# Optimization experiments

Hardware: AMD Instinct MI355X
Metric: run time of the kernel (lower is better)

## Reference

```python
import jax, jax.numpy as jnp
import numpy as np

B, T, N, D_IN = 2, 64, 64, 512
HID, L, H = 256, 2, 4
C = HID // H  # 64 per-head channels
NEG_SLOPE = 0.2
LN_EPS = 1e-5


def setup_inputs() -> dict:
    key = jax.random.key(0)
    ks = jax.random.split(key, 8)
    s_in = 1.0 / np.sqrt(D_IN)
    s_h = 1.0 / np.sqrt(HID)
    s_c = 1.0 / np.sqrt(C)
    return {
        "x": jax.random.normal(ks[0], (B, T, N, D_IN), jnp.float32),
        "person_mask": jax.random.randint(ks[1], (B, T, N), 0, 2) > 0,
        "W_in": (jax.random.normal(ks[2], (D_IN, HID)) * s_in).astype(jnp.float32),
        "b_in": jnp.zeros((HID,), jnp.float32),
        "Wl": (jax.random.normal(ks[3], (L, HID, HID)) * s_h).astype(jnp.float32),
        "bl": jnp.zeros((L, HID), jnp.float32),
        "Wr": (jax.random.normal(ks[4], (L, HID, HID)) * s_h).astype(jnp.float32),
        "br": jnp.zeros((L, HID), jnp.float32),
        "att": (jax.random.normal(ks[5], (L, H, C)) * s_c).astype(jnp.float32),
        "out_bias": jnp.zeros((L, HID), jnp.float32),
        "ln_scale": jnp.ones((L, HID), jnp.float32),
        "ln_bias": jnp.zeros((L, HID), jnp.float32),
    }


def _layernorm(x, g, b):
    mu = jnp.mean(x, axis=-1, keepdims=True)
    var = jnp.mean(jnp.square(x - mu), axis=-1, keepdims=True)
    return (x - mu) * jax.lax.rsqrt(var + LN_EPS) * g + b


def _gatv2_layer(h, allowed, Wl, bl, Wr, br, att, ob):
    # h: [bt, N, HID]; allowed: [bt, N, N] bool (edge j->i at [b,i,j])
    bt, n, _ = h.shape
    xl = (h @ Wl + bl).reshape(bt, n, H, C)  # source features (messages)
    xr = (h @ Wr + br).reshape(bt, n, H, C)  # target features
    # GATv2 logit: e_ij = a . leaky_relu(xr_i + xl_j), per head
    s = xr[:, :, None, :, :] + xl[:, None, :, :, :]  # [bt, i, j, H, C]
    e = jnp.einsum('bijhc,hc->bijh', jax.nn.leaky_relu(s, NEG_SLOPE), att)
    e = jnp.where(allowed[..., None], e, -1e9)
    alpha = jax.nn.softmax(e, axis=2)  # segment softmax over incoming edges j
    out = jnp.einsum('bijh,bjhc->bihc', alpha, xl)  # weighted scatter-sum
    return out.reshape(bt, n, H * C) + ob


def _forward(x, person_mask, W_in, b_in, Wl, bl, Wr, br, att, out_bias, ln_scale, ln_bias):
    b, t, n, _ = x.shape
    bt = b * t
    h = (x @ W_in + b_in).reshape(bt, n, HID)
    m = person_mask.reshape(bt, n)
    # edges: all pairs among masked nodes (incl. diag) + self loops for every node
    allowed = (m[:, :, None] & m[:, None, :]) | jnp.eye(n, dtype=bool)[None]
    hi = h
    for li in range(L):
        res = hi
        g = _gatv2_layer(hi, allowed, Wl[li], bl[li], Wr[li], br[li], att[li], out_bias[li])
        g = jax.nn.elu(g)  # dropout is identity in eval mode
        g = _layernorm(g, ln_scale[li], ln_bias[li])
        hi = g + res  # use_residual=True
        hi = jnp.where(m[:, :, None], hi, 0.0)
    # graphs with <=1 masked node are skipped (pass through projected features)
    keep = (jnp.sum(m, axis=-1) > 1)[:, None, None]
    out = jnp.where(keep, hi, h)
    return out.reshape(b, t, n, HID)


def reference(x, person_mask, W_in, b_in, Wl, bl, Wr, br, att, out_bias, ln_scale, ln_bias):
    return _forward(x, person_mask, W_in, b_in, Wl, bl, Wr, br, att, out_bias, ln_scale, ln_bias)
```

## Files before the change

kernel.cpp:

```cpp
#include <hip/hip_runtime.h>
#include <hip/hip_bf16.h>

#define BT_G   128
#define NND    64
#define D_IN_  512
#define HID_   256
#define NH     4
#define NCH    64
#define NROWS  8192
#define LN_EPS_    1e-5f

typedef __hip_bfloat16 bf16;
typedef __attribute__((ext_vector_type(8))) short short8;
typedef __attribute__((ext_vector_type(4))) float float4v;

__device__ __forceinline__ float toF(bf16 x) { return __bfloat162float(x); }

__global__ __launch_bounds__(256) void transpose_all_kernel(
    const float* __restrict__ W_in, const float* __restrict__ Wl,
    const float* __restrict__ Wr, const unsigned int* __restrict__ mw,
    bf16* __restrict__ WTin, bf16* __restrict__ WlrT, int* __restrict__ mout) {
    const int z = blockIdx.z;
    const int tid = threadIdx.x;
    if (z == 5) {
        if (blockIdx.x || blockIdx.y) return;
        __shared__ int okInt, okF32, okB16, okByte;
        if (tid == 0) { okInt = 1; okF32 = 1; okB16 = 1; okByte = 1; }
        __syncthreads();
        int aI = 1, aF = 1, aB = 1, aC = 1;
        for (int i = tid; i < 2048; i += 256) {
            unsigned w = mw[i];
            aI &= (w <= 1u);
            aF &= (w == 0u || w == 0x3F800000u);
            unsigned lo = w & 0xFFFFu, hi = w >> 16;
            aB &= ((lo == 0u || lo == 0x3F80u) && (hi == 0u || hi == 0x3F80u));
            aC &= (((w | (w >> 8) | (w >> 16) | (w >> 24)) & 0xFEu) == 0u);
        }
        if (!aI) atomicAnd(&okInt, 0);
        if (!aF) atomicAnd(&okF32, 0);
        if (!aB) atomicAnd(&okB16, 0);
        if (!aC) atomicAnd(&okByte, 0);
        __syncthreads();
        const int layout = (okInt || okF32) ? 0 : (okB16 ? 2 : (okByte ? 3 : 0));
        for (int i = tid; i < NROWS; i += 256) {
            int v;
            if (layout == 2)      v = (((const unsigned short*)mw)[i] != 0);
            else if (layout == 3) v = (((const unsigned char*)mw)[i] != 0);
            else                  v = (mw[i] != 0u);
            mout[i] = v;
        }
        return;
    }
    __shared__ float t[32][33];
    const float* src; bf16* dst; int K;
    if (z == 0)      { src = W_in;                 dst = WTin;                    K = 512; }
    else if (z <= 2) { src = Wl + (z - 1) * 65536; dst = WlrT + (z - 1) * 131072; K = 256; }
    else             { src = Wr + (z - 3) * 65536; dst = WlrT + (z - 3) * 131072 + 256 * 256; K = 256; }
    const int n0 = blockIdx.x * 32, k0 = blockIdx.y * 32;
    if (k0 >= K) return;
    const int tx = tid & 31, ty = tid >> 5;
    #pragma unroll
    for (int i = 0; i < 4; ++i)
        t[ty + 8 * i][tx] = src[(size_t)(k0 + ty + 8 * i) * 256 + n0 + tx];
    __syncthreads();
    #pragma unroll
    for (int i = 0; i < 4; ++i)
        dst[(size_t)(n0 + ty + 8 * i) * K + k0 + tx] =
            __float2bfloat16(t[tx][ty + 8 * i]);
}

__global__ __launch_bounds__(256) void gemm_in_kernel(
    const float* __restrict__ A, const bf16* __restrict__ BT,
    const float* __restrict__ bias, float* __restrict__ Cf,
    bf16* __restrict__ Cb16)
{
    __shared__ bf16 As[64 * 72];
    __shared__ bf16 Bs[64 * 72];
    const int tid  = threadIdx.x;
    const int wave = tid >> 6, lane = tid & 63;
    const int quad = lane >> 4, l16 = lane & 15;
    const int m0 = blockIdx.y * 64, n0 = blockIdx.x * 64;
    const int wm = (wave & 1) * 32, wn = (wave >> 1) * 32;
    float4v acc[2][2] = {};
    const int r  = tid >> 2;
    const int cq = (tid & 3) * 16;

    for (int k0 = 0; k0 < D_IN_; k0 += 64) {
        const float* sa = A + (size_t)(m0 + r) * D_IN_ + k0 + cq;
        const float4 f0 = *(const float4*)(sa);
        const float4 f1 = *(const float4*)(sa + 4);
        const float4 f2 = *(const float4*)(sa + 8);
        const float4 f3 = *(const float4*)(sa + 12);
        const bf16* sb = BT + (size_t)(n0 + r) * D_IN_ + k0 + cq;
        const float4 b0 = *(const float4*)(sb);
        const float4 b1 = *(const float4*)(sb + 8);
        union { bf16 h[16]; float4 v[2]; } u;
        u.h[0]=__float2bfloat16(f0.x); u.h[1]=__float2bfloat16(f0.y);
        u.h[2]=__float2bfloat16(f0.z); u.h[3]=__float2bfloat16(f0.w);
        u.h[4]=__float2bfloat16(f1.x); u.h[5]=__float2bfloat16(f1.y);
        u.h[6]=__float2bfloat16(f1.z); u.h[7]=__float2bfloat16(f1.w);
        u.h[8]=__float2bfloat16(f2.x); u.h[9]=__float2bfloat16(f2.y);
        u.h[10]=__float2bfloat16(f2.z); u.h[11]=__float2bfloat16(f2.w);
        u.h[12]=__float2bfloat16(f3.x); u.h[13]=__float2bfloat16(f3.y);
        u.h[14]=__float2bfloat16(f3.z); u.h[15]=__float2bfloat16(f3.w);
        __syncthreads();
        *(float4*)(&As[r * 72 + cq])     = u.v[0];
        *(float4*)(&As[r * 72 + cq + 8]) = u.v[1];
        *(float4*)(&Bs[r * 72 + cq])     = b0;
        *(float4*)(&Bs[r * 72 + cq + 8]) = b1;
        __syncthreads();
        #pragma unroll
        for (int kk = 0; kk < 64; kk += 32) {
            short8 af[2], bf2[2];
            #pragma unroll
            for (int mi = 0; mi < 2; ++mi)
                af[mi] = *(const short8*)(&As[(wm + mi * 16 + l16) * 72 + kk + quad * 8]);
            #pragma unroll
            for (int ni = 0; ni < 2; ++ni)
                bf2[ni] = *(const short8*)(&Bs[(wn + ni * 16 + l16) * 72 + kk + quad * 8]);
            #pragma unroll
            for (int mi = 0; mi < 2; ++mi)
                #pragma unroll
                for (int ni = 0; ni < 2; ++ni)
                    acc[mi][ni] = __builtin_amdgcn_mfma_f32_16x16x32_bf16(
                        af[mi], bf2[ni], acc[mi][ni], 0, 0, 0);
        }
    }
    #pragma unroll
    for (int ni = 0; ni < 2; ++ni) {
        const int col = n0 + wn + ni * 16 + l16;
        const float bv = bias[col];
        #pragma unroll
        for (int mi = 0; mi < 2; ++mi)
            #pragma unroll
            for (int rr = 0; rr < 4; ++rr) {
                const int row = m0 + wm + mi * 16 + quad * 4 + rr;
                const float v = acc[mi][ni][rr] + bv;
                Cf[(size_t)row * HID_ + col] = v;
                Cb16[(size_t)row * HID_ + col] = __float2bfloat16(v);
            }
    }
}

__global__ __launch_bounds__(256) void gemm_mfma_kernel(
    const bf16* __restrict__ A, const bf16* __restrict__ BT,
    const float* __restrict__ bias0, const float* __restrict__ bias1,
    float* __restrict__ Ca, float* __restrict__ Cbf, int M, int K)
{
    __shared__ bf16 As[128 * 72];
    __shared__ bf16 Bs[64 * 72];
    const int tid  = threadIdx.x;
    const int wave = tid >> 6, lane = tid & 63;
    const int quad = lane >> 4, l16 = lane & 15;
    const int m0 = blockIdx.y * 128, n0g = blockIdx.x * 64;
    const int wm = (wave & 1) * 64, wn = (wave >> 1) * 32;
    float4v acc[4][2] = {};
    const int r  = tid >> 2;
    const int cq = (tid & 3) * 16;

    for (int k0 = 0; k0 < K; k0 += 64) {
        const bf16* sa0 = A  + (size_t)(m0 + r) * K + k0 + cq;
        const bf16* sa1 = sa0 + (size_t)64 * K;
        const bf16* sb  = BT + (size_t)(n0g + r) * K + k0 + cq;
        const float4 a00 = *(const float4*)(sa0);
        const float4 a01 = *(const float4*)(sa0 + 8);
        const float4 a10 = *(const float4*)(sa1);
        const float4 a11 = *(const float4*)(sa1 + 8);
        const float4 b0  = *(const float4*)(sb);
        const float4 b1  = *(const float4*)(sb + 8);
        __syncthreads();
        *(float4*)(&As[r * 72 + cq])            = a00;
        *(float4*)(&As[r * 72 + cq + 8])        = a01;
        *(float4*)(&As[(r + 64) * 72 + cq])     = a10;
        *(float4*)(&As[(r + 64) * 72 + cq + 8]) = a11;
        *(float4*)(&Bs[r * 72 + cq])            = b0;
        *(float4*)(&Bs[r * 72 + cq + 8])        = b1;
        __syncthreads();
        #pragma unroll
        for (int kk = 0; kk < 64; kk += 32) {
            short8 af[4], bf2[2];
            #pragma unroll
            for (int mi = 0; mi < 4; ++mi)
                af[mi] = *(const short8*)(&As[(wm + mi * 16 + l16) * 72 + kk + quad * 8]);
            #pragma unroll
            for (int ni = 0; ni < 2; ++ni)
                bf2[ni] = *(const short8*)(&Bs[(wn + ni * 16 + l16) * 72 + kk + quad * 8]);
            #pragma unroll
            for (int mi = 0; mi < 4; ++mi)
                #pragma unroll
                for (int ni = 0; ni < 2; ++ni)
                    acc[mi][ni] = __builtin_amdgcn_mfma_f32_16x16x32_bf16(
                        af[mi], bf2[ni], acc[mi][ni], 0, 0, 0);
        }
    }
    const bool loHalf = (n0g < 256);
    float* Co = loHalf ? Ca : Cbf;
    const float* bp = loHalf ? bias0 : bias1;
    const int cbase = loHalf ? n0g : (n0g - 256);
    #pragma unroll
    for (int ni = 0; ni < 2; ++ni) {
        const int col = cbase + wn + ni * 16 + l16;
        const float bv = bp[col];
        #pragma unroll
        for (int mi = 0; mi < 4; ++mi)
            #pragma unroll
            for (int rr = 0; rr < 4; ++rr) {
                const int row = m0 + wm + mi * 16 + quad * 4 + rr;
                Co[(size_t)row * 256 + col] = acc[mi][ni][rr] + bv;
            }
    }
}

__global__ __launch_bounds__(256) void attn_kernel(
    const float* xl, const float* xr, const float* att,
    const int* msk, float* g)
{
    __shared__ float xls [64][68];
    __shared__ float xlsT[64][68];
    __shared__ float xrsT[64][68];
    __shared__ float esT [64][68];
    __shared__ float av[64], P[64], Q[64], mxf[64], inv[64];
    __shared__ float pmax[4][64], psum[4][64];
    __shared__ int   ms[64];
    const int tid  = threadIdx.x;
    const int head = blockIdx.x, gr = blockIdx.y;
    const int ti = tid >> 4, tj = tid & 15;
    const int i0 = ti * 4, j0 = tj * 4;
    const float* xlg = xl + (size_t)gr * NND * HID_ + head * NCH;
    const float* xrg = xr + (size_t)gr * NND * HID_ + head * NCH;

    {
        const int r  = tid >> 2;
        const int c0 = (tid & 3) * 16;
        float a[4][4], b[4][4];
        #pragma unroll
        for (int k = 0; k < 4; ++k) {
            *(float4*)a[k] = *(const float4*)(xlg + r * HID_ + c0 + 4 * k);
            *(float4*)b[k] = *(const float4*)(xrg + r * HID_ + c0 + 4 * k);
        }
        #pragma unroll
        for (int k = 0; k < 4; ++k)
            *(float4*)&xls[r][c0 + 4 * k] = *(float4*)a[k];
        #pragma unroll
        for (int k = 0; k < 4; ++k)
            #pragma unroll
            for (int w = 0; w < 4; ++w) {
                xlsT[c0 + 4 * k + w][r] = a[k][w];
                xrsT[c0 + 4 * k + w][r] = b[k][w];
            }
    }
    if (tid < 64) {
        av[tid] = att[head * NCH + tid];
        ms[tid] = msk[gr * NND + tid];
    }
    __syncthreads();

    float aa[4][4] = {};
    for (int c = 0; c < 64; ++c) {
        float xr4[4], xl4[4];
        *(float4*)xr4 = *(const float4*)&xrsT[c][i0];
        *(float4*)xl4 = *(const float4*)&xlsT[c][j0];
        const float a = av[c];
        #pragma unroll
        for (int y = 0; y < 4; ++y)
            #pragma unroll
            for (int x = 0; x < 4; ++x)
                aa[y][x] = fmaf(a, fabsf(xr4[y] + xl4[x]), aa[y][x]);
    }
    if (tid < 64) {
        float s = 0.f;
        for (int c = 0; c < 64; ++c) s = fmaf(av[c], xrsT[c][tid], s);
        P[tid] = s;
    } else if (tid < 128) {
        const int j = tid - 64;
        float s = 0.f;
        for (int c = 0; c < 64; ++c) s = fmaf(av[c], xlsT[c][j], s);
        Q[j] = s;
    }
    __syncthreads();

    {
        float Pv[4], Qv[4]; int mi4[4], mj4[4];
        #pragma unroll
        for (int y = 0; y < 4; ++y) { Pv[y] = P[i0 + y]; mi4[y] = ms[i0 + y]; }
        #pragma unroll
        for (int x = 0; x < 4; ++x) { Qv[x] = Q[j0 + x]; mj4[x] = ms[j0 + x]; }
        #pragma unroll
        for (int x = 0; x < 4; ++x) {
            float col[4];
            #pragma unroll
            for (int y = 0; y < 4; ++y) {
                float e = fmaf(0.4f, aa[y][x], 0.6f * (Pv[y] + Qv[x]));
                const bool allowed = (mi4[y] && mj4[x]) || (i0 + y == j0 + x);
                col[y] = allowed ? e : -1e9f;
            }
            *(float4*)&esT[j0 + x][i0] = *(float4*)col;
        }
    }
    __syncthreads();

    {
        const int si = tid & 63, q = tid >> 6;
        float mx = -1e30f;
        #pragma unroll
        for (int k = 0; k < 16; ++k) mx = fmaxf(mx, esT[16 * q + k][si]);
        pmax[q][si] = mx;
    }
    __syncthreads();
    if (tid < 64)
        mxf[tid] = fmaxf(fmaxf(pmax[0][tid], pmax[1][tid]),
                         fmaxf(pmax[2][tid], pmax[3][tid]));
    __syncthreads();
    {
        const int si = tid & 63, q = tid >> 6;
        const float mx = mxf[si];
        float s = 0.f;
        #pragma unroll
        for (int k = 0; k < 16; ++k) {
            const float ev = __expf(esT[16 * q + k][si] - mx);
            esT[16 * q + k][si] = ev;
            s += ev;
        }
        psum[q][si] = s;
    }
    __syncthreads();
    if (tid < 64)
        inv[tid] = 1.f / (psum[0][tid] + psum[1][tid] + psum[2][tid] + psum[3][tid]);
    __syncthreads();

    {
        const int c0 = j0;
        float oa[4][4] = {};
        for (int j = 0; j < 64; ++j) {
            float al[4], xv[4];
            *(float4*)al = *(const float4*)&esT[j][i0];
            *(float4*)xv = *(const float4*)&xls[j][c0];
            #pragma unroll
            for (int y = 0; y < 4; ++y)
                #pragma unroll
                for (int x = 0; x < 4; ++x)
                    oa[y][x] = fmaf(al[y], xv[x], oa[y][x]);
        }
        #pragma unroll
        for (int y = 0; y < 4; ++y) {
            const float iv = inv[i0 + y];
            float o[4];
            #pragma unroll
            for (int x = 0; x < 4; ++x) o[x] = oa[y][x] * iv;
            float* go = g + (size_t)(gr * NND + i0 + y) * HID_ + head * NCH + c0;
            *(float4*)go = *(float4*)o;
        }
    }
}

__global__ __launch_bounds__(256) void epilogue_kernel(
    const float* __restrict__ g, const float* res,
    const float* __restrict__ ob, const float* __restrict__ lns,
    const float* __restrict__ lnb, const int* __restrict__ msk,
    float* hout, bf16* hb, int finalSel)
{
    const int lane = threadIdx.x & 63;
    const int wave = threadIdx.x >> 6;
    const int m = blockIdx.x * 4 + wave;
    if (finalSel) {
        const int gr = m >> 6;
        const int mv = msk[gr * NND + lane];
        const unsigned long long bal = __ballot(mv != 0);
        if (__popcll(bal) <= 1) return;
    }
    const float* grow = g + (size_t)m * HID_;
    float v[4];
    float sum = 0.f;
    #pragma unroll
    for (int q = 0; q < 4; ++q) {
        const int c = q * 64 + lane;
        float x = grow[c] + ob[c];
        x = x > 0.f ? x : (__expf(x) - 1.f);
        v[q] = x; sum += x;
    }
    #pragma unroll
    for (int off = 1; off < 64; off <<= 1) sum += __shfl_xor(sum, off);
    const float mu = sum * (1.f / 256.f);
    float vs = 0.f;
    #pragma unroll
    for (int q = 0; q < 4; ++q) { const float d = v[q] - mu; vs += d * d; }
    #pragma unroll
    for (int off = 1; off < 64; off <<= 1) vs += __shfl_xor(vs, off);
    const float rstd = rsqrtf(vs * (1.f / 256.f) + LN_EPS_);
    const int mnode = msk[m];
    const float* rrow = res + (size_t)m * HID_;
    float* ho = hout + (size_t)m * HID_;
    #pragma unroll
    for (int q = 0; q < 4; ++q) {
        const int c = q * 64 + lane;
        float y = (v[q] - mu) * rstd * lns[c] + lnb[c];
        y += rrow[c];
        y = mnode ? y : 0.f;
        ho[c] = y;
        if (hb) hb[(size_t)m * HID_ + c] = __float2bfloat16(y);
    }
}

extern "C" void kernel_launch(void* const* d_in, const int* in_sizes, int n_in,
                              void* d_out, int out_size, void* d_ws, size_t ws_size,
                              hipStream_t stream) {
    const float* x    = (const float*)d_in[0];
    const float* W_in = (const float*)d_in[2];
    const float* b_in = (const float*)d_in[3];
    const float* Wl   = (const float*)d_in[4];
    const float* bl   = (const float*)d_in[5];
    const float* Wr   = (const float*)d_in[6];
    const float* br   = (const float*)d_in[7];
    const float* att  = (const float*)d_in[8];
    const float* ob   = (const float*)d_in[9];
    const float* lns  = (const float*)d_in[10];
    const float* lnb  = (const float*)d_in[11];
    float* out = (float*)d_out;

    char* w = (char*)d_ws;
    int*   mcan = (int*)w;                      w += 32768;
    float* h    = (float*)w;                    w += (size_t)NROWS * HID_ * 4;
    float* xlb  = (float*)w;                    w += (size_t)NROWS * HID_ * 4;
    float* xrb  = (float*)w;                    w += (size_t)NROWS * HID_ * 4;
    bf16*  hxb  = (bf16*)w;                     w += (size_t)NROWS * HID_ * 2;
    bf16*  WTin = (bf16*)w;                     w += (size_t)D_IN_ * HID_ * 2;
    bf16*  WlrT = (bf16*)w;
    float* gb   = xrb;

    transpose_all_kernel<<<dim3(8, 16, 6), 256, 0, stream>>>(
        W_in, Wl, Wr, (const unsigned int*)d_in[1], WTin, WlrT, mcan);

    gemm_in_kernel<<<dim3(HID_ / 64, NROWS / 64), 256, 0, stream>>>(
        x, WTin, b_in, out, hxb);

    for (int li = 0; li < 2; ++li) {
        const float* resf = (li == 0) ? out : h;
        gemm_mfma_kernel<<<dim3(512 / 64, NROWS / 128), 256, 0, stream>>>(
            hxb, WlrT + (size_t)li * 512 * HID_, bl + li * HID_, br + li * HID_,
            xlb, xrb, NROWS, HID_);
        attn_kernel<<<dim3(NH, BT_G), 256, 0, stream>>>(
            xlb, xrb, att + li * NH * NCH, mcan, gb);
        if (li == 0) {
            epilogue_kernel<<<NROWS / 4, 256, 0, stream>>>(
                gb, resf, ob, lns, lnb, mcan, h, hxb, 0);
        } else {
            epilogue_kernel<<<NROWS / 4, 256, 0, stream>>>(
                gb, resf, ob + HID_, lns + HID_, lnb + HID_, mcan,
                out, (bf16*)nullptr, 1);
        }
    }

    (void)in_sizes; (void)n_in; (void)out_size; (void)ws_size;
}
```

Measured before the change: 177.4 us.

## Fuse GATv2 attention with ELU/LayerNorm epilogue, looping heads per block

Merges the attention kernel and the ELU/LayerNorm/residual epilogue into one kernel. Each block now handles 32 target rows of one graph and loops over all four heads, keeping the per-head outputs in shared memory and then normalising each row in place. This drops the global round trip of the attention output and one kernel launch per layer. In exchange the grid is halved to 256 blocks, each doing serial per-head work with many barriers. Shared-memory use rises to roughly 87 KB per block, and source features are loaded twice per graph.

```diff
diff --git a/kernel.cpp b/kernel.cpp
--- a/kernel.cpp
+++ b/kernel.cpp
@@ -211,193 +211,211 @@
     }
 }
 
-__global__ __launch_bounds__(256) void attn_kernel(
-    const float* xl, const float* xr, const float* att,
-    const int* msk, float* g)
+__global__ __launch_bounds__(256) void attn_ep_kernel(
+    const float* __restrict__ xl, const float* __restrict__ xr,
+    const float* __restrict__ att, const int* __restrict__ msk,
+    const float* __restrict__ res, const float* __restrict__ ob,
+    const float* __restrict__ lns, const float* __restrict__ lnb,
+    float* __restrict__ hout, bf16* __restrict__ hb, int finalSel)
 {
     __shared__ float xls [64][68];
     __shared__ float xlsT[64][68];
-    __shared__ float xrsT[64][68];
-    __shared__ float esT [64][68];
-    __shared__ float av[64], P[64], Q[64], mxf[64], inv[64];
-    __shared__ float pmax[4][64], psum[4][64];
+    __shared__ float xrsT[64][36];
+    __shared__ float esT [64][36];
+    __shared__ float gsh [32][264];
+    __shared__ float av[64], P[32], Q[64], mxf[32], inv[32];
+    __shared__ float pmax[8][32], psum[8][32];
     __shared__ int   ms[64];
-    const int tid  = threadIdx.x;
-    const int head = blockIdx.x, gr = blockIdx.y;
+    __shared__ int   keepFlag;
+
+    const int tid   = threadIdx.x;
+    const int half  = blockIdx.x;
+    const int gr    = blockIdx.y;
+    const int ibase = half * 32;
     const int ti = tid >> 4, tj = tid & 15;
-    const int i0 = ti * 4, j0 = tj * 4;
-    const float* xlg = xl + (size_t)gr * NND * HID_ + head * NCH;
-    const float* xrg = xr + (size_t)gr * NND * HID_ + head * NCH;
-
-    {
-        const int r  = tid >> 2;
-        const int c0 = (tid & 3) * 16;
-        float a[4][4], b[4][4];
-        #pragma unroll
-        for (int k = 0; k < 4; ++k) {
-            *(float4*)a[k] = *(const float4*)(xlg + r * HID_ + c0 + 4 * k);
-            *(float4*)b[k] = *(const float4*)(xrg + r * HID_ + c0 + 4 * k);
-        }
-        #pragma unroll
-        for (int k = 0; k < 4; ++k)
-            *(float4*)&xls[r][c0 + 4 * k] = *(float4*)a[k];
-        #pragma unroll
-        for (int k = 0; k < 4; ++k)
-            #pragma unroll
-            for (int w = 0; w < 4; ++w) {
-                xlsT[c0 + 4 * k + w][r] = a[k][w];
-                xrsT[c0 + 4 * k + w][r] = b[k][w];
-            }
-    }
-    if (tid < 64) {
-        av[tid] = att[head * NCH + tid];
-        ms[tid] = msk[gr * NND + tid];
-    }
+    const int i0 = ti * 2, j0 = tj * 4;
+
+    if (tid < 64) ms[tid] = msk[gr * NND + tid];
     __syncthreads();
-
-    float aa[4][4] = {};
-    for (int c = 0; c < 64; ++c) {
-        float xr4[4], xl4[4];
-        *(float4*)xr4 = *(const float4*)&xrsT[c][i0];
-        *(float4*)xl4 = *(const float4*)&xlsT[c][j0];
-        const float a = av[c];
-        #pragma unroll
-        for (int y = 0; y < 4; ++y)
-            #pragma unroll
-            for (int x = 0; x < 4; ++x)
-                aa[y][x] = fmaf(a, fabsf(xr4[y] + xl4[x]), aa[y][x]);
-    }
-    if (tid < 64) {
-        float s = 0.f;
-        for (int c = 0; c < 64; ++c) s = fmaf(av[c], xrsT[c][tid], s);
-        P[tid] = s;
-    } else if (tid < 128) {
-        const int j = tid - 64;
-        float s = 0.f;
-        for (int c = 0; c < 64; ++c) s = fmaf(av[c], xlsT[c][j], s);
-        Q[j] = s;
+    if (tid == 0) {
+        int s = 0;
+        #pragma unroll
+        for (int k = 0; k < 64; ++k) s += (ms[k] != 0);
+        keepFlag = (s > 1);
+    }
+
+    for (int head = 0; head < NH; ++head) {
+        const float* xlg = xl + (size_t)gr * NND * HID_ + head * NCH;
+        const float* xrg = xr + ((size_t)gr * NND + ibase) * HID_ + head * NCH;
+        {
+            const int r  = tid >> 2;
+            const int c0 = (tid & 3) * 16;
+            const int r2 = tid >> 3;
+            const int cb = (tid & 7) * 8;
+            float a[4][4], b[2][4];
+            #pragma unroll
+            for (int k = 0; k < 4; ++k)
+                *(float4*)a[k] = *(const float4*)(xlg + r * HID_ + c0 + 4 * k);
+            *(float4*)b[0] = *(const float4*)(xrg + r2 * HID_ + cb);
+            *(float4*)b[1] = *(const float4*)(xrg + r2 * HID_ + cb + 4);
+            __syncthreads();
+            #pragma unroll
+            for (int k = 0; k < 4; ++k)
+                *(float4*)&xls[r][c0 + 4 * k] = *(float4*)a[k];
+            #pragma unroll
+            for (int k = 0; k < 4; ++k)
+                #pragma unroll
+                for (int w = 0; w < 4; ++w)
+                    xlsT[c0 + 4 * k + w][r] = a[k][w];
+            #pragma unroll
+            for (int k = 0; k < 2; ++k)
+                #pragma unroll
+                for (int w = 0; w < 4; ++w)
+                    xrsT[cb + 4 * k + w][r2] = b[k][w];
+            if (tid < 64) av[tid] = att[head * NCH + tid];
+        }
+        __syncthreads();
+
+        float aa[2][4] = {};
+        for (int c = 0; c < 64; ++c) {
+            const float a = av[c];
+            const float2 xr2 = *(const float2*)&xrsT[c][i0];
+            const float4 xl4 = *(const float4*)&xlsT[c][j0];
+            const float xrv[2] = {xr2.x, xr2.y};
+            const float xlv[4] = {xl4.x, xl4.y, xl4.z, xl4.w};
+            #pragma unroll
+            for (int y = 0; y < 2; ++y)
+                #pragma unroll
+                for (int x = 0; x < 4; ++x)
+                    aa[y][x] = fmaf(a, fabsf(xrv[y] + xlv[x]), aa[y][x]);
+        }
+        if (tid < 32) {
+            float s = 0.f;
+            for (int c = 0; c < 64; ++c) s = fmaf(av[c], xrsT[c][tid], s);
+            P[tid] = s;
+        } else if (tid >= 64 && tid < 128) {
+            const int j = tid - 64;
+            float s = 0.f;
+            for (int c = 0; c < 64; ++c) s = fmaf(av[c], xlsT[c][j], s);
+            Q[j] = s;
+        }
+        __syncthreads();
+
+        {
+            float Pv[2], Qv[4]; int mi2[2], mj4[4];
+            #pragma unroll
+            for (int y = 0; y < 2; ++y) { Pv[y] = P[i0 + y]; mi2[y] = ms[ibase + i0 + y]; }
+            #pragma unroll
+            for (int x = 0; x < 4; ++x) { Qv[x] = Q[j0 + x]; mj4[x] = ms[j0 + x]; }
+            #pragma unroll
+            for (int x = 0; x < 4; ++x) {
+                float col[2];
+                #pragma unroll
+                for (int y = 0; y < 2; ++y) {
+                    float e = fmaf(0.4f, aa[y][x], 0.6f * (Pv[y] + Qv[x]));
+                    const bool allowed = (mi2[y] && mj4[x]) || (ibase + i0 + y == j0 + x);
+                    col[y] = allowed ? e : -1e9f;
+                }
+                *(float2*)&esT[j0 + x][i0] = *(float2*)col;
+            }
+        }
+        __syncthreads();
+
+        {
+            const int si = tid & 31, q = tid >> 5;
+            float mx = -1e30f;
+            #pragma unroll
+            for (int k = 0; k < 8; ++k) mx = fmaxf(mx, esT[8 * q + k][si]);
+            pmax[q][si] = mx;
+        }
+        __syncthreads();
+        if (tid < 32) {
+            float m = pmax[0][tid];
+            #pragma unroll
+            for (int q = 1; q < 8; ++q) m = fmaxf(m, pmax[q][tid]);
+            mxf[tid] = m;
+        }
+        __syncthreads();
+        {
+            const int si = tid & 31, q = tid >> 5;
+            const float mx = mxf[si];
+            float s = 0.f;
+            #pragma unroll
+            for (int k = 0; k < 8; ++k) {
+                const float ev = __expf(esT[8 * q + k][si] - mx);
+                esT[8 * q + k][si] = ev;
+                s += ev;
+            }
+            psum[q][si] = s;
+        }
+        __syncthreads();
+        if (tid < 32) {
+            float s = psum[0][tid];
+            #pragma unroll
+            for (int q = 1; q < 8; ++q) s += psum[q][tid];
+            inv[tid] = 1.f / s;
+        }
+        __syncthreads();
+
+        {
+            float oa[2][4] = {};
+            for (int j = 0; j < 64; ++j) {
+                const float2 al = *(const float2*)&esT[j][i0];
+                const float4 xv = *(const float4*)&xls[j][j0];
+                const float alv[2] = {al.x, al.y};
+                const float xvv[4] = {xv.x, xv.y, xv.z, xv.w};
+                #pragma unroll
+                for (int y = 0; y < 2; ++y)
+                    #pragma unroll
+                    for (int x = 0; x < 4; ++x)
+                        oa[y][x] = fmaf(alv[y], xvv[x], oa[y][x]);
+            }
+            #pragma unroll
+            for (int y = 0; y < 2; ++y) {
+                const float iv = inv[i0 + y];
+                float o[4];
+                #pragma unroll
+                for (int x = 0; x < 4; ++x) o[x] = oa[y][x] * iv;
+                *(float4*)&gsh[i0 + y][head * NCH + j0] = *(float4*)o;
+            }
+        }
     }
     __syncthreads();
 
-    {
-        float Pv[4], Qv[4]; int mi4[4], mj4[4];
-        #pragma unroll
-        for (int y = 0; y < 4; ++y) { Pv[y] = P[i0 + y]; mi4[y] = ms[i0 + y]; }
-        #pragma unroll
-        for (int x = 0; x < 4; ++x) { Qv[x] = Q[j0 + x]; mj4[x] = ms[j0 + x]; }
-        #pragma unroll
-        for (int x = 0; x < 4; ++x) {
-            float col[4];
-            #pragma unroll
-            for (int y = 0; y < 4; ++y) {
-                float e = fmaf(0.4f, aa[y][x], 0.6f * (Pv[y] + Qv[x]));
-                const bool allowed = (mi4[y] && mj4[x]) || (i0 + y == j0 + x);
-                col[y] = allowed ? e : -1e9f;
-            }
-            *(float4*)&esT[j0 + x][i0] = *(float4*)col;
-        }
-    }
-    __syncthreads();
-
-    {
-        const int si = tid & 63, q = tid >> 6;
-        float mx = -1e30f;
-        #pragma unroll
-        for (int k = 0; k < 16; ++k) mx = fmaxf(mx, esT[16 * q + k][si]);
-        pmax[q][si] = mx;
-    }
-    __syncthreads();
-    if (tid < 64)
-        mxf[tid] = fmaxf(fmaxf(pmax[0][tid], pmax[1][tid]),
-                         fmaxf(pmax[2][tid], pmax[3][tid]));
-    __syncthreads();
-    {
-        const int si = tid & 63, q = tid >> 6;
-        const float mx = mxf[si];
-        float s = 0.f;
-        #pragma unroll
-        for (int k = 0; k < 16; ++k) {
-            const float ev = __expf(esT[16 * q + k][si] - mx);
-            esT[16 * q + k][si] = ev;
-            s += ev;
-        }
-        psum[q][si] = s;
-    }
-    __syncthreads();
-    if (tid < 64)
-        inv[tid] = 1.f / (psum[0][tid] + psum[1][tid] + psum[2][tid] + psum[3][tid]);
-    __syncthreads();
-
-    {
-        const int c0 = j0;
-        float oa[4][4] = {};
-        for (int j = 0; j < 64; ++j) {
-            float al[4], xv[4];
-            *(float4*)al = *(const float4*)&esT[j][i0];
-            *(float4*)xv = *(const float4*)&xls[j][c0];
-            #pragma unroll
-            for (int y = 0; y < 4; ++y)
-                #pragma unroll
-                for (int x = 0; x < 4; ++x)
-                    oa[y][x] = fmaf(al[y], xv[x], oa[y][x]);
-        }
-        #pragma unroll
-        for (int y = 0; y < 4; ++y) {
-            const float iv = inv[i0 + y];
-            float o[4];
-            #pragma unroll
-            for (int x = 0; x < 4; ++x) o[x] = oa[y][x] * iv;
-            float* go = g + (size_t)(gr * NND + i0 + y) * HID_ + head * NCH + c0;
-            *(float4*)go = *(float4*)o;
-        }
-    }
-}
-
-__global__ __launch_bounds__(256) void epilogue_kernel(
-    const float* __restrict__ g, const float* res,
-    const float* __restrict__ ob, const float* __restrict__ lns,
-    const float* __restrict__ lnb, const int* __restrict__ msk,
-    float* hout, bf16* hb, int finalSel)
-{
-    const int lane = threadIdx.x & 63;
-    const int wave = threadIdx.x >> 6;
-    const int m = blockIdx.x * 4 + wave;
-    if (finalSel) {
-        const int gr = m >> 6;
-        const int mv = msk[gr * NND + lane];
-        const unsigned long long bal = __ballot(mv != 0);
-        if (__popcll(bal) <= 1) return;
-    }
-    const float* grow = g + (size_t)m * HID_;
-    float v[4];
-    float sum = 0.f;
-    #pragma unroll
-    for (int q = 0; q < 4; ++q) {
-        const int c = q * 64 + lane;
-        float x = grow[c] + ob[c];
-        x = x > 0.f ? x : (__expf(x) - 1.f);
-        v[q] = x; sum += x;
-    }
-    #pragma unroll
-    for (int off = 1; off < 64; off <<= 1) sum += __shfl_xor(sum, off);
-    const float mu = sum * (1.f / 256.f);
-    float vs = 0.f;
-    #pragma unroll
-    for (int q = 0; q < 4; ++q) { const float d = v[q] - mu; vs += d * d; }
-    #pragma unroll
-    for (int off = 1; off < 64; off <<= 1) vs += __shfl_xor(vs, off);
-    const float rstd = rsqrtf(vs * (1.f / 256.f) + LN_EPS_);
-    const int mnode = msk[m];
-    const float* rrow = res + (size_t)m * HID_;
-    float* ho = hout + (size_t)m * HID_;
-    #pragma unroll
-    for (int q = 0; q < 4; ++q) {
-        const int c = q * 64 + lane;
-        float y = (v[q] - mu) * rstd * lns[c] + lnb[c];
-        y += rrow[c];
-        y = mnode ? y : 0.f;
-        ho[c] = y;
-        if (hb) hb[(size_t)m * HID_ + c] = __float2bfloat16(y);
+    if (finalSel && !keepFlag) return;
+    const int lane = tid & 63, wave = tid >> 6;
+    for (int rr = wave; rr < 32; rr += 4) {
+        const int m = gr * NND + ibase + rr;
+        float v[4];
+        float sum = 0.f;
+        #pragma unroll
+        for (int q = 0; q < 4; ++q) {
+            const int c = q * 64 + lane;
+            float x = gsh[rr][c] + ob[c];
+            x = x > 0.f ? x : (__expf(x) - 1.f);
+            v[q] = x; sum += x;
+        }
+        #pragma unroll
+        for (int off = 1; off < 64; off <<= 1) sum += __shfl_xor(sum, off);
+        const float mu = sum * (1.f / 256.f);
+        float vs = 0.f;
+        #pragma unroll
+        for (int q = 0; q < 4; ++q) { const float d = v[q] - mu; vs += d * d; }
+        #pragma unroll
+        for (int off = 1; off < 64; off <<= 1) vs += __shfl_xor(vs, off);
+        const float rstd = rsqrtf(vs * (1.f / 256.f) + LN_EPS_);
+        const int mnode = ms[ibase + rr];
+        const float* rrow = res + (size_t)m * HID_;
+        float* ho = hout + (size_t)m * HID_;
+        #pragma unroll
+        for (int q = 0; q < 4; ++q) {
+            const int c = q * 64 + lane;
+            float y = (v[q] - mu) * rstd * lns[c] + lnb[c];
+            y += rrow[c];
+            y = mnode ? y : 0.f;
+            ho[c] = y;
+            if (hb) hb[(size_t)m * HID_ + c] = __float2bfloat16(y);
+        }
     }
 }
 
@@ -425,7 +443,6 @@
     bf16*  hxb  = (bf16*)w;                     w += (size_t)NROWS * HID_ * 2;
     bf16*  WTin = (bf16*)w;                     w += (size_t)D_IN_ * HID_ * 2;
     bf16*  WlrT = (bf16*)w;
-    float* gb   = xrb;
 
     transpose_all_kernel<<<dim3(8, 16, 6), 256, 0, stream>>>(
         W_in, Wl, Wr, (const unsigned int*)d_in[1], WTin, WlrT, mcan);
@@ -438,15 +455,13 @@
         gemm_mfma_kernel<<<dim3(512 / 64, NROWS / 128), 256, 0, stream>>>(
             hxb, WlrT + (size_t)li * 512 * HID_, bl + li * HID_, br + li * HID_,
             xlb, xrb, NROWS, HID_);
-        attn_kernel<<<dim3(NH, BT_G), 256, 0, stream>>>(
-            xlb, xrb, att + li * NH * NCH, mcan, gb);
         if (li == 0) {
-            epilogue_kernel<<<NROWS / 4, 256, 0, stream>>>(
-                gb, resf, ob, lns, lnb, mcan, h, hxb, 0);
+            attn_ep_kernel<<<dim3(2, BT_G), 256, 0, stream>>>(
+                xlb, xrb, att, mcan, resf, ob, lns, lnb, h, hxb, 0);
         } else {
-            epilogue_kernel<<<NROWS / 4, 256, 0, stream>>>(
-                gb, resf, ob + HID_, lns + HID_, lnb + HID_, mcan,
-                out, (bf16*)nullptr, 1);
+            attn_ep_kernel<<<dim3(2, BT_G), 256, 0, stream>>>(
+                xlb, xrb, att + NH * NCH, mcan, resf, ob + HID_, lns + HID_,
+                lnb + HID_, out, (bf16*)nullptr, 1);
         }
     }
 
```

After: 212.2 us. 19.6% more time.

## Fuse ELU+LayerNorm epilogue into attention kernel via last-block atomic counter

Applied to the files above, without the earlier changes.

Removes the separate epilogue kernel launch. Each of the four head blocks for a graph bumps a per-graph atomic counter, and the last one to finish runs ELU, LayerNorm, residual add and masking for that graph's 64 rows. This saves a launch and its scheduling gap per layer. In exchange it adds threadfence and atomic overhead, and the epilogue now runs on only 128 blocks, which may lower parallelism in that phase.

```diff
diff --git a/kernel.cpp b/kernel.cpp
--- a/kernel.cpp
+++ b/kernel.cpp
@@ -19,11 +19,13 @@
 __global__ __launch_bounds__(256) void transpose_all_kernel(
     const float* __restrict__ W_in, const float* __restrict__ Wl,
     const float* __restrict__ Wr, const unsigned int* __restrict__ mw,
-    bf16* __restrict__ WTin, bf16* __restrict__ WlrT, int* __restrict__ mout) {
+    bf16* __restrict__ WTin, bf16* __restrict__ WlrT, int* __restrict__ mout,
+    int* __restrict__ cnt) {
     const int z = blockIdx.z;
     const int tid = threadIdx.x;
     if (z == 5) {
         if (blockIdx.x || blockIdx.y) return;
+        if (tid < 256) cnt[tid] = 0;
         __shared__ int okInt, okF32, okB16, okByte;
         if (tid == 0) { okInt = 1; okF32 = 1; okB16 = 1; okByte = 1; }
         __syncthreads();
@@ -213,7 +215,11 @@
 
 __global__ __launch_bounds__(256) void attn_kernel(
     const float* xl, const float* xr, const float* att,
-    const int* msk, float* g)
+    const int* msk, float* g,
+    int* __restrict__ cnt, const float* __restrict__ res,
+    const float* __restrict__ ob, const float* __restrict__ lns,
+    const float* __restrict__ lnb, float* __restrict__ hout,
+    bf16* __restrict__ hb, int finalSel)
 {
     __shared__ float xls [64][68];
     __shared__ float xlsT[64][68];
@@ -222,6 +228,7 @@
     __shared__ float av[64], P[64], Q[64], mxf[64], inv[64];
     __shared__ float pmax[4][64], psum[4][64];
     __shared__ int   ms[64];
+    __shared__ int   lastF;
     const int tid  = threadIdx.x;
     const int head = blockIdx.x, gr = blockIdx.y;
     const int ti = tid >> 4, tj = tid & 15;
@@ -351,53 +358,55 @@
             *(float4*)go = *(float4*)o;
         }
     }
-}
-
-__global__ __launch_bounds__(256) void epilogue_kernel(
-    const float* __restrict__ g, const float* res,
-    const float* __restrict__ ob, const float* __restrict__ lns,
-    const float* __restrict__ lnb, const int* __restrict__ msk,
-    float* hout, bf16* hb, int finalSel)
-{
-    const int lane = threadIdx.x & 63;
-    const int wave = threadIdx.x >> 6;
-    const int m = blockIdx.x * 4 + wave;
+
+    __syncthreads();
+    if (tid == 0) {
+        __threadfence();
+        lastF = (atomicAdd(&cnt[gr], 1) == 3);
+    }
+    __syncthreads();
+    if (!lastF) return;
+    __threadfence();
     if (finalSel) {
-        const int gr = m >> 6;
-        const int mv = msk[gr * NND + lane];
-        const unsigned long long bal = __ballot(mv != 0);
-        if (__popcll(bal) <= 1) return;
-    }
-    const float* grow = g + (size_t)m * HID_;
-    float v[4];
-    float sum = 0.f;
-    #pragma unroll
-    for (int q = 0; q < 4; ++q) {
-        const int c = q * 64 + lane;
-        float x = grow[c] + ob[c];
-        x = x > 0.f ? x : (__expf(x) - 1.f);
-        v[q] = x; sum += x;
-    }
-    #pragma unroll
-    for (int off = 1; off < 64; off <<= 1) sum += __shfl_xor(sum, off);
-    const float mu = sum * (1.f / 256.f);
-    float vs = 0.f;
-    #pragma unroll
-    for (int q = 0; q < 4; ++q) { const float d = v[q] - mu; vs += d * d; }
-    #pragma unroll
-    for (int off = 1; off < 64; off <<= 1) vs += __shfl_xor(vs, off);
-    const float rstd = rsqrtf(vs * (1.f / 256.f) + LN_EPS_);
-    const int mnode = msk[m];
-    const float* rrow = res + (size_t)m * HID_;
-    float* ho = hout + (size_t)m * HID_;
-    #pragma unroll
-    for (int q = 0; q < 4; ++q) {
-        const int c = q * 64 + lane;
-        float y = (v[q] - mu) * rstd * lns[c] + lnb[c];
-        y += rrow[c];
-        y = mnode ? y : 0.f;
-        ho[c] = y;
-        if (hb) hb[(size_t)m * HID_ + c] = __float2bfloat16(y);
+        int s = 0;
+        #pragma unroll
+        for (int k = 0; k < 64; ++k) s += (ms[k] != 0);
+        if (s <= 1) return;
+    }
+    const int lane = tid & 63, wv = tid >> 6;
+    for (int rr = wv; rr < 64; rr += 4) {
+        const int m = gr * NND + rr;
+        const float* grow = g + (size_t)m * HID_;
+        float v[4];
+        float sum = 0.f;
+        #pragma unroll
+        for (int q = 0; q < 4; ++q) {
+            const int c = q * 64 + lane;
+            float x = grow[c] + ob[c];
+            x = x > 0.f ? x : (__expf(x) - 1.f);
+            v[q] = x; sum += x;
+        }
+        #pragma unroll
+        for (int off = 1; off < 64; off <<= 1) sum += __shfl_xor(sum, off);
+        const float mu = sum * (1.f / 256.f);
+        float vs = 0.f;
+        #pragma unroll
+        for (int q = 0; q < 4; ++q) { const float d = v[q] - mu; vs += d * d; }
+        #pragma unroll
+        for (int off = 1; off < 64; off <<= 1) vs += __shfl_xor(vs, off);
+        const float rstd = rsqrtf(vs * (1.f / 256.f) + LN_EPS_);
+        const int mnode = ms[rr];
+        const float* rrow = res + (size_t)m * HID_;
+        float* ho = hout + (size_t)m * HID_;
+        #pragma unroll
+        for (int q = 0; q < 4; ++q) {
+            const int c = q * 64 + lane;
+            float y = (v[q] - mu) * rstd * lns[c] + lnb[c];
+            y += rrow[c];
+            y = mnode ? y : 0.f;
+            ho[c] = y;
+            if (hb) hb[(size_t)m * HID_ + c] = __float2bfloat16(y);
+        }
     }
 }
 
@@ -419,6 +428,7 @@
 
     char* w = (char*)d_ws;
     int*   mcan = (int*)w;                      w += 32768;
+    int*   cnt  = (int*)w;                      w += 1024;
     float* h    = (float*)w;                    w += (size_t)NROWS * HID_ * 4;
     float* xlb  = (float*)w;                    w += (size_t)NROWS * HID_ * 4;
     float* xrb  = (float*)w;                    w += (size_t)NROWS * HID_ * 4;
@@ -428,7 +438,7 @@
     float* gb   = xrb;
 
     transpose_all_kernel<<<dim3(8, 16, 6), 256, 0, stream>>>(
-        W_in, Wl, Wr, (const unsigned int*)d_in[1], WTin, WlrT, mcan);
+        W_in, Wl, Wr, (const unsigned int*)d_in[1], WTin, WlrT, mcan, cnt);
 
     gemm_in_kernel<<<dim3(HID_ / 64, NROWS / 64), 256, 0, stream>>>(
         x, WTin, b_in, out, hxb);
@@ -438,14 +448,14 @@
         gemm_mfma_kernel<<<dim3(512 / 64, NROWS / 128), 256, 0, stream>>>(
             hxb, WlrT + (size_t)li * 512 * HID_, bl + li * HID_, br + li * HID_,
             xlb, xrb, NROWS, HID_);
-        attn_kernel<<<dim3(NH, BT_G), 256, 0, stream>>>(
-            xlb, xrb, att + li * NH * NCH, mcan, gb);
         if (li == 0) {
-            epilogue_kernel<<<NROWS / 4, 256, 0, stream>>>(
-                gb, resf, ob, lns, lnb, mcan, h, hxb, 0);
+            attn_kernel<<<dim3(NH, BT_G), 256, 0, stream>>>(
+                xlb, xrb, att, mcan, gb,
+                cnt, resf, ob, lns, lnb, h, hxb, 0);
         } else {
-            epilogue_kernel<<<NROWS / 4, 256, 0, stream>>>(
-                gb, resf, ob + HID_, lns + HID_, lnb + HID_, mcan,
+            attn_kernel<<<dim3(NH, BT_G), 256, 0, stream>>>(
+                xlb, xrb, att + NH * NCH, mcan, gb,
+                cnt + 128, resf, ob + HID_, lns + HID_, lnb + HID_,
                 out, (bf16*)nullptr, 1);
         }
     }
```

Measured after the change: 269.0 us. 51.6% more time.
